# Performance work log

Measured on AMD Instinct MI355X. Metric: run time of the kernel, lower is better.

The kernel has to match this reference:

```python
import jax, jax.numpy as jnp
import numpy as np

B = 64        # batch_size (graphs)
N_HITS = 1024 # nodes per graph
D = 64        # input_dim == output_dim (hidden)
E = 16 * B * N_HITS // 16 * 16  # 1,048,576 edges (16 per node avg)


def setup_inputs() -> dict:
    key = jax.random.key(0)
    ks = jax.random.split(key, 12)
    x = jax.random.normal(ks[0], (B * N_HITS, D), dtype=jnp.float32)
    # edges constrained within each graph (PyG-style batched edge_index)
    g = jax.random.randint(ks[1], (E,), 0, B)
    s_loc = jax.random.randint(ks[2], (E,), 0, N_HITS)
    e_loc = jax.random.randint(ks[3], (E,), 0, N_HITS)
    edge_index = jnp.stack([g * N_HITS + s_loc, g * N_HITS + e_loc], axis=0).astype(jnp.int64)
    batch = jnp.repeat(jnp.arange(B, dtype=jnp.int64), N_HITS)  # node -> graph id
    s = 0.05
    return {
        "x": x,
        "edge_index": edge_index,
        "batch": batch,
        "batch_size": B,
        "weight": jax.random.normal(ks[4], (D, D), dtype=jnp.float32) * s,
        "bias": jax.random.normal(ks[5], (D,), dtype=jnp.float32) * s,
        "w1": jax.random.normal(ks[6], (D, D), dtype=jnp.float32) * s,
        "b1": jax.random.normal(ks[7], (D,), dtype=jnp.float32) * s,
        "w2": jax.random.normal(ks[8], (D, D), dtype=jnp.float32) * s,
        "b2": jax.random.normal(ks[9], (D,), dtype=jnp.float32) * s,
        "w3": jax.random.normal(ks[10], (D, 1), dtype=jnp.float32) * s,
        "b3": jax.random.normal(ks[11], (1,), dtype=jnp.float32) * s,
    }


def reference(x, edge_index, batch, batch_size, weight, bias, w1, b1, w2, b2, w3, b3):
    n_hits = x.shape[0] // batch_size
    nodes = x.reshape(batch_size, n_hits, x.shape[1])  # [B, n, d]
    start, end = edge_index[0], edge_index[1]
    g = batch[start]
    # dense adjacency scatter: A[g, start_local, end_local] = 1.0 (is_e=False branch)
    A = jnp.zeros((batch_size, n_hits, n_hits), dtype=x.dtype)
    A = A.at[g, start - n_hits * g, end - n_hits * g].set(1.0)
    # GraphConv: y = (A @ x) @ W + bias
    y = jnp.einsum('bij,bjd->bid', A, nodes)
    y = y @ weight + bias  # [B, n, d]
    # agg='max': torch.max(nodes, dim=1)[0] -> values
    pooled = jnp.max(y, axis=1)  # [B, d]
    # MLP: Linear-Tanh-Linear-Tanh-Linear
    h = jnp.tanh(pooled @ w1 + b1)
    h = jnp.tanh(h @ w2 + b2)
    return h @ w3 + b3  # [B, 1] logits
```

## Files before the change

### kernel.cpp

```cpp
#include <hip/hip_runtime.h>
#include <hip/hip_bf16.h>


#define NNODES 65536
#define NGRAPH 64
#define NLOCAL 1024
#define DIM 64
#define MASK_WORDS 32
#define KMAX 64
#define CHUNK_ROWS 256
#define NBIN 256
#define NBUCKET 256
#define SEGCAP 64

__device__ __forceinline__ unsigned f2ord(float f) {
    unsigned u = __float_as_uint(f);
    return (u & 0x80000000u) ? ~u : (u | 0x80000000u);
}
__device__ __forceinline__ float ord2f(unsigned u) {
    return (u & 0x80000000u) ? __uint_as_float(u & 0x7FFFFFFFu)
                             : __uint_as_float(~u);
}

__global__ __launch_bounds__(256) void clear_kernel(uint4* __restrict__ p, int n4)
{
    int i = blockIdx.x * 256 + threadIdx.x;
    int stride = gridDim.x * 256;
    uint4 z = {0u, 0u, 0u, 0u};
    for (; i < n4; i += stride) p[i] = z;
}

__global__ __launch_bounds__(256) void bin_kernel(
    const int* __restrict__ ei, int E,
    unsigned* __restrict__ seg, unsigned short* __restrict__ segcnt)
{
    __shared__ unsigned off[NBUCKET];
    int tid = threadIdx.x;
    off[tid] = 0u;
    __syncthreads();
    int perblk = (E + NBIN - 1) / NBIN;
    int e0 = blockIdx.x * perblk;
    int e1 = min(e0 + perblk, E);
    unsigned* myseg = seg + (size_t)blockIdx.x * NBUCKET * SEGCAP;
    for (int e = e0 + tid; e < e1; e += 256) {
        int s = ei[e];
        int t = ei[E + e] & (NLOCAL - 1);
        int sl = s & (NLOCAL - 1);
        int bk = ((s >> 10) << 2) | (sl >> 8);
        unsigned slot = atomicAdd(&off[bk], 1u);
        if (slot < SEGCAP) myseg[bk * SEGCAP + slot] = (unsigned)((sl << 10) | t);
    }
    __syncthreads();
    unsigned c = off[tid];
    segcnt[blockIdx.x * NBUCKET + tid] = (unsigned short)(c < SEGCAP ? c : SEGCAP);
}

__global__ __launch_bounds__(256) void xw_kernel(
    const float* __restrict__ x, const float* __restrict__ W,
    float* __restrict__ xw)
{
    __shared__ float4 xlds[64 * 16];
    int tid = threadIdx.x;
    int row0 = blockIdx.x * 64;
    const float4* xg4 = (const float4*)(x + (size_t)row0 * DIM);
    for (int i = tid; i < 64 * 16; i += 256) xlds[i] = xg4[i];
    int col = tid & 63;
    int rg  = tid >> 6;
    float w[64];
    #pragma unroll
    for (int k = 0; k < 64; ++k) w[k] = W[k * DIM + col];
    __syncthreads();
    #pragma unroll
    for (int rr = 0; rr < 16; ++rr) {
        int row = rg * 16 + rr;
        float acc = 0.f;
        #pragma unroll
        for (int k4 = 0; k4 < 16; ++k4) {
            float4 xv = xlds[row * 16 + k4];
            acc = fmaf(xv.x, w[4 * k4 + 0], acc);
            acc = fmaf(xv.y, w[4 * k4 + 1], acc);
            acc = fmaf(xv.z, w[4 * k4 + 2], acc);
            acc = fmaf(xv.w, w[4 * k4 + 3], acc);
        }
        xw[(size_t)(row0 + row) * DIM + col] = acc;
    }
}

__global__ __launch_bounds__(1024) void agg_fused_kernel(
    const float* __restrict__ xw, const float* __restrict__ bias,
    const unsigned* __restrict__ seg, const unsigned short* __restrict__ segcnt,
    unsigned* __restrict__ pooled_u)
{
    __shared__ unsigned mask[CHUNK_ROWS * MASK_WORDS];
    __shared__ unsigned short rowcnt[CHUNK_ROWS];
    __shared__ float red[16 * DIM];

    int tid = threadIdx.x;
    int lane = tid & 63, wave = tid >> 6;
    int b = blockIdx.x;
    int g = ((b >> 5) << 3) | (b & 7);
    int chunk = (b >> 3) & 3;
    int bk = (g << 2) | chunk;

    for (int i = tid; i < CHUNK_ROWS * MASK_WORDS; i += 1024) mask[i] = 0u;
    __syncthreads();

    for (int idx = tid; idx < NBIN * SEGCAP; idx += 1024) {
        int sb = idx >> 6;
        int sl = idx & 63;
        int n = segcnt[sb * NBUCKET + bk];
        if (sl < n) {
            unsigned pk = seg[((size_t)sb * NBUCKET + bk) * SEGCAP + sl];
            int r = (pk >> 10) & (CHUNK_ROWS - 1);
            int t = pk & (NLOCAL - 1);
            atomicOr(&mask[r * MASK_WORDS + (t >> 5)], 1u << (t & 31));
        }
    }
    __syncthreads();

    const float* xwg = xw + ((size_t)g << 10) * DIM;
    float bv = bias[lane];
    float vmax = -INFINITY;
    unsigned short* lists = (unsigned short*)mask;

    for (int i = 0; i < 16; ++i) {
        int row = wave * 16 + i;
        unsigned bits = 0u; int c = 0;
        if (lane < 32) { bits = mask[row * MASK_WORDS + lane]; c = __popc(bits); }
        int inc = c;
        #pragma unroll
        for (int d = 1; d < 32; d <<= 1) {
            int v = __shfl_up(inc, d, 32);
            if ((lane & 31) >= d) inc += v;
        }
        if (lane < 32) {
            int off = inc - c;
            unsigned short* lr = lists + row * KMAX;
            while (bits) {
                int bb = __ffs(bits) - 1;
                bits &= bits - 1;
                if (off < KMAX) lr[off] = (unsigned short)(lane * 32 + bb);
                ++off;
            }
            if (lane == 31) rowcnt[row] = (unsigned short)(inc < KMAX ? inc : KMAX);
        }
        __syncthreads();
        int cc = rowcnt[row];
        const unsigned* lr32 = (const unsigned*)(lists + row * KMAX);
        float a0 = 0.f, a1 = 0.f, a2 = 0.f, a3 = 0.f;
        float a4 = 0.f, a5 = 0.f, a6 = 0.f, a7 = 0.f;
        int j = 0;
        for (; j + 8 <= cc; j += 8) {
            unsigned p0 = lr32[(j >> 1) + 0], p1 = lr32[(j >> 1) + 1];
            unsigned p2 = lr32[(j >> 1) + 2], p3 = lr32[(j >> 1) + 3];
            a0 += xwg[(p0 & 0xFFFF) * DIM + lane];
            a1 += xwg[(p0 >> 16) * DIM + lane];
            a2 += xwg[(p1 & 0xFFFF) * DIM + lane];
            a3 += xwg[(p1 >> 16) * DIM + lane];
            a4 += xwg[(p2 & 0xFFFF) * DIM + lane];
            a5 += xwg[(p2 >> 16) * DIM + lane];
            a6 += xwg[(p3 & 0xFFFF) * DIM + lane];
            a7 += xwg[(p3 >> 16) * DIM + lane];
        }
        for (; j + 4 <= cc; j += 4) {
            unsigned p0 = lr32[(j >> 1) + 0], p1 = lr32[(j >> 1) + 1];
            a0 += xwg[(p0 & 0xFFFF) * DIM + lane];
            a1 += xwg[(p0 >> 16) * DIM + lane];
            a2 += xwg[(p1 & 0xFFFF) * DIM + lane];
            a3 += xwg[(p1 >> 16) * DIM + lane];
        }
        const unsigned short* lr = lists + row * KMAX;
        for (; j < cc; ++j) a0 += xwg[(int)lr[j] * DIM + lane];
        float s = ((a0 + a1) + (a2 + a3)) + ((a4 + a5) + (a6 + a7)) + bv;
        vmax = fmaxf(vmax, s);
        __syncthreads();
    }

    red[wave * DIM + lane] = vmax;
    __syncthreads();
    if (wave == 0) {
        float m = red[lane];
        #pragma unroll
        for (int w = 1; w < 16; ++w) m = fmaxf(m, red[w * DIM + lane]);
        atomicMax(&pooled_u[g * DIM + lane], f2ord(m));
    }
}

__global__ __launch_bounds__(64) void mlp_kernel(
    const unsigned* __restrict__ pooled_u,
    const float* __restrict__ w1, const float* __restrict__ b1,
    const float* __restrict__ w2, const float* __restrict__ b2,
    const float* __restrict__ w3, const float* __restrict__ b3,
    float* __restrict__ out)
{
    __shared__ float buf[DIM];
    __shared__ float buf2[DIM];
    int g = blockIdx.x, l = threadIdx.x;
    buf[l] = ord2f(pooled_u[g * DIM + l]);
    __syncthreads();
    float h = b1[l];
    for (int k = 0; k < DIM; ++k) h = fmaf(buf[k], w1[k * DIM + l], h);
    buf2[l] = tanhf(h);
    __syncthreads();
    float h2 = b2[l];
    for (int k = 0; k < DIM; ++k) h2 = fmaf(buf2[k], w2[k * DIM + l], h2);
    h2 = tanhf(h2);
    float v = h2 * w3[l];
    #pragma unroll
    for (int off = 32; off; off >>= 1) v += __shfl_down(v, off, 64);
    if (l == 0) out[g] = v + b3[0];
}

__global__ __launch_bounds__(256) void scatter_kernel(
    const int* __restrict__ ei, unsigned* __restrict__ mask, int E)
{
    int e = blockIdx.x * 256 + threadIdx.x;
    if (e >= E) return;
    int start = ei[e];
    int col   = ei[E + e] & (NLOCAL - 1);
    atomicOr(&mask[(size_t)start * MASK_WORDS + (col >> 5)], 1u << (col & 31));
}

__global__ __launch_bounds__(256) void agg_kernel(
    const float* __restrict__ x, const float* __restrict__ weight,
    const float* __restrict__ bias, const unsigned* __restrict__ mask,
    unsigned* __restrict__ pooled_u)
{
    __shared__ float Wlds[DIM * DIM];
    __shared__ float blds[DIM];
    int tid = threadIdx.x;
    for (int i = tid; i < DIM * DIM; i += 256) Wlds[i] = weight[i];
    if (tid < DIM) blds[tid] = bias[tid];
    __syncthreads();
    int lane = tid & 63;
    int wave = tid >> 6;
    int rowbase = blockIdx.x * 64 + wave * 16;
    int g = rowbase >> 10;
    const float* xg = x + ((size_t)g << 10) * DIM;
    float vmax = -INFINITY;
    for (int rr = 0; rr < 16; ++rr) {
        int row = rowbase + rr;
        const unsigned* mrow = mask + (size_t)row * MASK_WORDS;
        float acc = 0.f;
        for (int w = 0; w < MASK_WORDS; ++w) {
            unsigned bits = mrow[w];
            while (bits) {
                int b = __ffs(bits) - 1;
                bits &= bits - 1;
                acc += xg[(size_t)(w * 32 + b) * DIM + lane];
            }
        }
        float y = blds[lane];
        for (int k = 0; k < DIM; ++k) {
            float a = __shfl(acc, k, 64);
            y = fmaf(a, Wlds[k * DIM + lane], y);
        }
        vmax = fmaxf(vmax, y);
    }
    atomicMax(&pooled_u[g * DIM + lane], f2ord(vmax));
}

__global__ __launch_bounds__(1024) void fused_kernel(
    const float* __restrict__ x, const int* __restrict__ ei, int E,
    const float* __restrict__ weight, const float* __restrict__ bias,
    const float* __restrict__ w1, const float* __restrict__ b1,
    const float* __restrict__ w2, const float* __restrict__ b2,
    const float* __restrict__ w3, const float* __restrict__ b3,
    float* __restrict__ out)
{
    __shared__ unsigned mask[CHUNK_ROWS * MASK_WORDS];
    __shared__ float Wlds[DIM * DIM];
    __shared__ float blds[DIM];
    __shared__ float red[16 * DIM];
    __shared__ float pool[DIM];
    __shared__ float hbuf[DIM];
    int tid = threadIdx.x;
    int g = blockIdx.x;
    int lane = tid & 63;
    int wave = tid >> 6;
    const float* xg = x + ((size_t)g << 10) * DIM;
    for (int i = tid; i < DIM * DIM; i += 1024) Wlds[i] = weight[i];
    if (tid < DIM) blds[tid] = bias[tid];
    float vmax = -INFINITY;
    for (int chunk = 0; chunk < NLOCAL / CHUNK_ROWS; ++chunk) {
        int row0 = chunk * CHUNK_ROWS;
        __syncthreads();
        for (int i = tid; i < CHUNK_ROWS * MASK_WORDS; i += 1024) mask[i] = 0u;
        __syncthreads();
        int lo = (g << 10) + row0, hi = lo + CHUNK_ROWS;
        for (int e = tid; e < E; e += 1024) {
            int s = ei[e];
            if (s >= lo && s < hi) {
                int t = ei[E + e] & (NLOCAL - 1);
                atomicOr(&mask[(s - lo) * MASK_WORDS + (t >> 5)], 1u << (t & 31));
            }
        }
        __syncthreads();
        for (int rr = 0; rr < CHUNK_ROWS / 16; ++rr) {
            int row = wave * (CHUNK_ROWS / 16) + rr;
            float acc = 0.f;
            for (int w = 0; w < MASK_WORDS; ++w) {
                unsigned bits = mask[row * MASK_WORDS + w];
                while (bits) {
                    int b = __ffs(bits) - 1;
                    bits &= bits - 1;
                    acc += xg[(size_t)(w * 32 + b) * DIM + lane];
                }
            }
            float y = blds[lane];
            for (int k = 0; k < DIM; ++k) {
                float a = __shfl(acc, k, 64);
                y = fmaf(a, Wlds[k * DIM + lane], y);
            }
            vmax = fmaxf(vmax, y);
        }
    }
    red[wave * DIM + lane] = vmax;
    __syncthreads();
    if (tid < DIM) {
        float m = red[tid];
        #pragma unroll
        for (int w = 1; w < 16; ++w) m = fmaxf(m, red[w * DIM + tid]);
        pool[tid] = m;
    }
    __syncthreads();
    if (tid < DIM) {
        float h = b1[tid];
        for (int k = 0; k < DIM; ++k) h = fmaf(pool[k], w1[k * DIM + tid], h);
        hbuf[tid] = tanhf(h);
    }
    __syncthreads();
    if (tid < DIM) {
        float h2 = b2[tid];
        for (int k = 0; k < DIM; ++k) h2 = fmaf(hbuf[k], w2[k * DIM + tid], h2);
        h2 = tanhf(h2);
        red[tid] = h2 * w3[tid];
    }
    __syncthreads();
    if (tid == 0) {
        float v = b3[0];
        for (int k = 0; k < DIM; ++k) v += red[k];
        out[g] = v;
    }
}

extern "C" void kernel_launch(void* const* d_in, const int* in_sizes, int n_in,
                              void* d_out, int out_size, void* d_ws, size_t ws_size,
                              hipStream_t stream)
{
    const float* x      = (const float*)d_in[0];
    const int*   ei     = (const int*)d_in[1];
    const float* weight = (const float*)d_in[4];
    const float* bias   = (const float*)d_in[5];
    const float* w1     = (const float*)d_in[6];
    const float* b1     = (const float*)d_in[7];
    const float* w2     = (const float*)d_in[8];
    const float* b2     = (const float*)d_in[9];
    const float* w3     = (const float*)d_in[10];
    const float* b3     = (const float*)d_in[11];
    float* out = (float*)d_out;

    const int E = in_sizes[1] / 2;

    const size_t PL_BYTES  = (size_t)NGRAPH * DIM * 4;
    const size_t SC_BYTES  = (size_t)NBIN * NBUCKET * 2;
    const size_t SEG_BYTES = (size_t)NBIN * NBUCKET * SEGCAP * 4;
    const size_t XW_BYTES  = (size_t)NNODES * DIM * 4;
    const size_t need_A = PL_BYTES + SC_BYTES + SEG_BYTES + XW_BYTES;
    const size_t MASKW  = (size_t)NNODES * MASK_WORDS;
    const size_t need_B = MASKW * 4 + PL_BYTES;

    if (d_ws != nullptr && ws_size >= need_A) {
        char* base = (char*)d_ws;
        unsigned*       pooled_u = (unsigned*)base;
        unsigned short* segcnt   = (unsigned short*)(base + PL_BYTES);
        unsigned*       seg      = (unsigned*)(base + PL_BYTES + SC_BYTES);
        float*          xw       = (float*)(base + PL_BYTES + SC_BYTES + SEG_BYTES);

        clear_kernel<<<4, 256, 0, stream>>>((uint4*)pooled_u, (int)(PL_BYTES / 16));
        bin_kernel<<<NBIN, 256, 0, stream>>>(ei, E, seg, segcnt);
        xw_kernel<<<NNODES / 64, 256, 0, stream>>>(x, weight, xw);
        agg_fused_kernel<<<NBUCKET, 1024, 0, stream>>>(xw, bias, seg, segcnt, pooled_u);
        mlp_kernel<<<NGRAPH, DIM, 0, stream>>>(pooled_u, w1, b1, w2, b2, w3, b3, out);
    } else if (d_ws != nullptr && ws_size >= need_B) {
        unsigned* mask     = (unsigned*)d_ws;
        unsigned* pooled_u = mask + MASKW;
        clear_kernel<<<1024, 256, 0, stream>>>((uint4*)mask, (int)((MASKW * 4 + PL_BYTES) / 16));
        scatter_kernel<<<(E + 255) / 256, 256, 0, stream>>>(ei, mask, E);
        agg_kernel<<<NNODES / 64, 256, 0, stream>>>(x, weight, bias, mask, pooled_u);
        mlp_kernel<<<NGRAPH, DIM, 0, stream>>>(pooled_u, w1, b1, w2, b2, w3, b3, out);
    } else {
        fused_kernel<<<NGRAPH, 1024, 0, stream>>>(
            x, ei, E, weight, bias, w1, b1, w2, b2, w3, b3, out);
    }
}
```

Baseline: 84.44 us.

## Halve aggregation chunk size, process two rows per wave without block syncs, fold clear into binning

Splits each graph into eight 128-row buckets instead of four 256-row ones, so the aggregation kernel launches 512 blocks with less LDS each, raising occupancy and parallelism. Each wave now builds neighbour lists for two rows at once, one per half-wave, and reads row counts through shuffles, which removes both per-row __syncthreads. The pooled-buffer clear moves into bin_kernel, dropping one kernel launch. Per-bucket segment capacity is halved to 32, which raises the risk of silently dropping edges if one bin holds more than 32 edges for a bucket.

```diff
diff --git a/kernel.cpp b/kernel.cpp
--- a/kernel.cpp
+++ b/kernel.cpp
@@ -8,10 +8,10 @@
 #define DIM 64
 #define MASK_WORDS 32
 #define KMAX 64
-#define CHUNK_ROWS 256
+#define CHUNK_ROWS 128
 #define NBIN 256
-#define NBUCKET 256
-#define SEGCAP 64
+#define NBUCKET 512
+#define SEGCAP 32
 
 __device__ __forceinline__ unsigned f2ord(float f) {
     unsigned u = __float_as_uint(f);
@@ -32,11 +32,14 @@
 
 __global__ __launch_bounds__(256) void bin_kernel(
     const int* __restrict__ ei, int E,
-    unsigned* __restrict__ seg, unsigned short* __restrict__ segcnt)
+    unsigned* __restrict__ seg, unsigned short* __restrict__ segcnt,
+    unsigned* __restrict__ pooled_u)
 {
     __shared__ unsigned off[NBUCKET];
     int tid = threadIdx.x;
     off[tid] = 0u;
+    off[tid + 256] = 0u;
+    if (blockIdx.x < 16) pooled_u[blockIdx.x * 256 + tid] = 0u;
     __syncthreads();
     int perblk = (E + NBIN - 1) / NBIN;
     int e0 = blockIdx.x * perblk;
@@ -46,13 +49,14 @@
         int s = ei[e];
         int t = ei[E + e] & (NLOCAL - 1);
         int sl = s & (NLOCAL - 1);
-        int bk = ((s >> 10) << 2) | (sl >> 8);
+        int bk = ((s >> 10) << 3) | (sl >> 7);
         unsigned slot = atomicAdd(&off[bk], 1u);
         if (slot < SEGCAP) myseg[bk * SEGCAP + slot] = (unsigned)((sl << 10) | t);
     }
     __syncthreads();
-    unsigned c = off[tid];
-    segcnt[blockIdx.x * NBUCKET + tid] = (unsigned short)(c < SEGCAP ? c : SEGCAP);
+    unsigned c0 = off[tid], c1 = off[tid + 256];
+    segcnt[blockIdx.x * NBUCKET + tid]       = (unsigned short)(c0 < SEGCAP ? c0 : SEGCAP);
+    segcnt[blockIdx.x * NBUCKET + tid + 256] = (unsigned short)(c1 < SEGCAP ? c1 : SEGCAP);
 }
 
 __global__ __launch_bounds__(256) void xw_kernel(
@@ -92,22 +96,21 @@
     unsigned* __restrict__ pooled_u)
 {
     __shared__ unsigned mask[CHUNK_ROWS * MASK_WORDS];
-    __shared__ unsigned short rowcnt[CHUNK_ROWS];
     __shared__ float red[16 * DIM];
 
     int tid = threadIdx.x;
     int lane = tid & 63, wave = tid >> 6;
     int b = blockIdx.x;
-    int g = ((b >> 5) << 3) | (b & 7);
-    int chunk = (b >> 3) & 3;
-    int bk = (g << 2) | chunk;
+    int g = ((b >> 6) << 3) | (b & 7);
+    int chunk = (b >> 3) & 7;
+    int bk = (g << 3) | chunk;
 
     for (int i = tid; i < CHUNK_ROWS * MASK_WORDS; i += 1024) mask[i] = 0u;
     __syncthreads();
 
     for (int idx = tid; idx < NBIN * SEGCAP; idx += 1024) {
-        int sb = idx >> 6;
-        int sl = idx & 63;
+        int sb = idx >> 5;
+        int sl = idx & 31;
         int n = segcnt[sb * NBUCKET + bk];
         if (sl < n) {
             unsigned pk = seg[((size_t)sb * NBUCKET + bk) * SEGCAP + sl];
@@ -123,57 +126,64 @@
     float vmax = -INFINITY;
     unsigned short* lists = (unsigned short*)mask;
 
-    for (int i = 0; i < 16; ++i) {
-        int row = wave * 16 + i;
-        unsigned bits = 0u; int c = 0;
-        if (lane < 32) { bits = mask[row * MASK_WORDS + lane]; c = __popc(bits); }
+    for (int i = 0; i < 8; i += 2) {
+        int rowa = wave * 8 + i;
+        int rowb = rowa + 1;
+        int myrow = (lane < 32) ? rowa : rowb;
+        unsigned bits = mask[myrow * MASK_WORDS + (lane & 31)];
+        int c = __popc(bits);
         int inc = c;
         #pragma unroll
         for (int d = 1; d < 32; d <<= 1) {
             int v = __shfl_up(inc, d, 32);
             if ((lane & 31) >= d) inc += v;
         }
-        if (lane < 32) {
+        {
             int off = inc - c;
-            unsigned short* lr = lists + row * KMAX;
+            unsigned short* lr = lists + myrow * KMAX;
             while (bits) {
                 int bb = __ffs(bits) - 1;
                 bits &= bits - 1;
-                if (off < KMAX) lr[off] = (unsigned short)(lane * 32 + bb);
+                if (off < KMAX) lr[off] = (unsigned short)((lane & 31) * 32 + bb);
                 ++off;
             }
-            if (lane == 31) rowcnt[row] = (unsigned short)(inc < KMAX ? inc : KMAX);
-        }
-        __syncthreads();
-        int cc = rowcnt[row];
-        const unsigned* lr32 = (const unsigned*)(lists + row * KMAX);
-        float a0 = 0.f, a1 = 0.f, a2 = 0.f, a3 = 0.f;
-        float a4 = 0.f, a5 = 0.f, a6 = 0.f, a7 = 0.f;
-        int j = 0;
-        for (; j + 8 <= cc; j += 8) {
-            unsigned p0 = lr32[(j >> 1) + 0], p1 = lr32[(j >> 1) + 1];
-            unsigned p2 = lr32[(j >> 1) + 2], p3 = lr32[(j >> 1) + 3];
-            a0 += xwg[(p0 & 0xFFFF) * DIM + lane];
-            a1 += xwg[(p0 >> 16) * DIM + lane];
-            a2 += xwg[(p1 & 0xFFFF) * DIM + lane];
-            a3 += xwg[(p1 >> 16) * DIM + lane];
-            a4 += xwg[(p2 & 0xFFFF) * DIM + lane];
-            a5 += xwg[(p2 >> 16) * DIM + lane];
-            a6 += xwg[(p3 & 0xFFFF) * DIM + lane];
-            a7 += xwg[(p3 >> 16) * DIM + lane];
-        }
-        for (; j + 4 <= cc; j += 4) {
-            unsigned p0 = lr32[(j >> 1) + 0], p1 = lr32[(j >> 1) + 1];
-            a0 += xwg[(p0 & 0xFFFF) * DIM + lane];
-            a1 += xwg[(p0 >> 16) * DIM + lane];
-            a2 += xwg[(p1 & 0xFFFF) * DIM + lane];
-            a3 += xwg[(p1 >> 16) * DIM + lane];
-        }
-        const unsigned short* lr = lists + row * KMAX;
-        for (; j < cc; ++j) a0 += xwg[(int)lr[j] * DIM + lane];
-        float s = ((a0 + a1) + (a2 + a3)) + ((a4 + a5) + (a6 + a7)) + bv;
-        vmax = fmaxf(vmax, s);
-        __syncthreads();
+        }
+        int cca = __shfl(inc, 31, 64);
+        int ccb = __shfl(inc, 63, 64);
+        cca = cca < KMAX ? cca : KMAX;
+        ccb = ccb < KMAX ? ccb : KMAX;
+        #pragma unroll
+        for (int half = 0; half < 2; ++half) {
+            int row = half ? rowb : rowa;
+            int cc = half ? ccb : cca;
+            const unsigned* lr32 = (const unsigned*)(lists + row * KMAX);
+            float a0 = 0.f, a1 = 0.f, a2 = 0.f, a3 = 0.f;
+            float a4 = 0.f, a5 = 0.f, a6 = 0.f, a7 = 0.f;
+            int j = 0;
+            for (; j + 8 <= cc; j += 8) {
+                unsigned p0 = lr32[(j >> 1) + 0], p1 = lr32[(j >> 1) + 1];
+                unsigned p2 = lr32[(j >> 1) + 2], p3 = lr32[(j >> 1) + 3];
+                a0 += xwg[(p0 & 0xFFFF) * DIM + lane];
+                a1 += xwg[(p0 >> 16) * DIM + lane];
+                a2 += xwg[(p1 & 0xFFFF) * DIM + lane];
+                a3 += xwg[(p1 >> 16) * DIM + lane];
+                a4 += xwg[(p2 & 0xFFFF) * DIM + lane];
+                a5 += xwg[(p2 >> 16) * DIM + lane];
+                a6 += xwg[(p3 & 0xFFFF) * DIM + lane];
+                a7 += xwg[(p3 >> 16) * DIM + lane];
+            }
+            for (; j + 2 <= cc; j += 2) {
+                unsigned p0 = lr32[j >> 1];
+                a0 += xwg[(p0 & 0xFFFF) * DIM + lane];
+                a1 += xwg[(p0 >> 16) * DIM + lane];
+            }
+            if (j < cc) {
+                unsigned p0 = lr32[j >> 1];
+                a0 += xwg[(p0 & 0xFFFF) * DIM + lane];
+            }
+            float s = ((a0 + a1) + (a2 + a3)) + ((a4 + a5) + (a6 + a7)) + bv;
+            vmax = fmaxf(vmax, s);
+        }
     }
 
     red[wave * DIM + lane] = vmax;
@@ -268,7 +278,7 @@
     const float* __restrict__ w3, const float* __restrict__ b3,
     float* __restrict__ out)
 {
-    __shared__ unsigned mask[CHUNK_ROWS * MASK_WORDS];
+    __shared__ unsigned mask[256 * MASK_WORDS];
     __shared__ float Wlds[DIM * DIM];
     __shared__ float blds[DIM];
     __shared__ float red[16 * DIM];
@@ -282,12 +292,12 @@
     for (int i = tid; i < DIM * DIM; i += 1024) Wlds[i] = weight[i];
     if (tid < DIM) blds[tid] = bias[tid];
     float vmax = -INFINITY;
-    for (int chunk = 0; chunk < NLOCAL / CHUNK_ROWS; ++chunk) {
-        int row0 = chunk * CHUNK_ROWS;
+    for (int chunk = 0; chunk < NLOCAL / 256; ++chunk) {
+        int row0 = chunk * 256;
         __syncthreads();
-        for (int i = tid; i < CHUNK_ROWS * MASK_WORDS; i += 1024) mask[i] = 0u;
+        for (int i = tid; i < 256 * MASK_WORDS; i += 1024) mask[i] = 0u;
         __syncthreads();
-        int lo = (g << 10) + row0, hi = lo + CHUNK_ROWS;
+        int lo = (g << 10) + row0, hi = lo + 256;
         for (int e = tid; e < E; e += 1024) {
             int s = ei[e];
             if (s >= lo && s < hi) {
@@ -296,8 +306,8 @@
             }
         }
         __syncthreads();
-        for (int rr = 0; rr < CHUNK_ROWS / 16; ++rr) {
-            int row = wave * (CHUNK_ROWS / 16) + rr;
+        for (int rr = 0; rr < 256 / 16; ++rr) {
+            int row = wave * (256 / 16) + rr;
             float acc = 0.f;
             for (int w = 0; w < MASK_WORDS; ++w) {
                 unsigned bits = mask[row * MASK_WORDS + w];
@@ -377,8 +387,7 @@
         unsigned*       seg      = (unsigned*)(base + PL_BYTES + SC_BYTES);
         float*          xw       = (float*)(base + PL_BYTES + SC_BYTES + SEG_BYTES);
 
-        clear_kernel<<<4, 256, 0, stream>>>((uint4*)pooled_u, (int)(PL_BYTES / 16));
-        bin_kernel<<<NBIN, 256, 0, stream>>>(ei, E, seg, segcnt);
+        bin_kernel<<<NBIN, 256, 0, stream>>>(ei, E, seg, segcnt, pooled_u);
         xw_kernel<<<NNODES / 64, 256, 0, stream>>>(x, weight, xw);
         agg_fused_kernel<<<NBUCKET, 1024, 0, stream>>>(xw, bias, seg, segcnt, pooled_u);
         mlp_kernel<<<NGRAPH, DIM, 0, stream>>>(pooled_u, w1, b1, w2, b2, w3, b3, out);
```

Measured after the change: 71.80 us. -15.0%, faster.
